# Kernel tuning notes

Hardware: AMD Instinct MI355X
Metric: run time of the kernel (lower is better)

The kernel has to match this reference:

```python
import jax, jax.numpy as jnp
import numpy as np

H = 16
D_MODEL = 1024
D_K = D_MODEL // H
NWORDS = 16384


def setup_inputs() -> dict:
    key0 = jax.random.key(0)
    ks = jax.random.split(key0, 11)
    s = 0.02
    return {
        "query": jax.random.normal(ks[0], (1, D_MODEL), dtype=jnp.float32),
        "key": jax.random.normal(ks[1], (NWORDS, D_MODEL), dtype=jnp.float32),
        "value": jax.random.normal(ks[2], (NWORDS, D_MODEL), dtype=jnp.float32),
        "Wq": jax.random.normal(ks[3], (D_MODEL, D_MODEL), dtype=jnp.float32) * s,
        "bq": jax.random.normal(ks[4], (D_MODEL,), dtype=jnp.float32) * s,
        "Wk": jax.random.normal(ks[5], (D_MODEL, D_MODEL), dtype=jnp.float32) * s,
        "bk": jax.random.normal(ks[6], (D_MODEL,), dtype=jnp.float32) * s,
        "Wv": jax.random.normal(ks[7], (D_MODEL, D_MODEL), dtype=jnp.float32) * s,
        "bv": jax.random.normal(ks[8], (D_MODEL,), dtype=jnp.float32) * s,
        "Wo": jax.random.normal(ks[9], (D_MODEL, D_MODEL), dtype=jnp.float32) * s,
        "bo": jax.random.normal(ks[10], (D_MODEL,), dtype=jnp.float32) * s,
    }


def reference(query, key, value, Wq, bq, Wk, bk, Wv, bv, Wo, bo):
    # torch Linear: y = x @ W.T + b
    q = (query @ Wq.T + bq).reshape(H, D_K)          # [h, d_k]  (single query token)
    k = (key @ Wk.T + bk).reshape(-1, H, D_K)        # [n, h, d_k]
    v = (value @ Wv.T + bv).reshape(-1, H, D_K)      # [n, h, d_k]
    # NOTE: original module applies NO 1/sqrt(d_k) scaling.
    scores = jnp.einsum("hd,nhd->hn", q, k)          # [h, n]
    p_attn = jax.nn.softmax(scores, axis=-1)          # dropout p=0 -> no-op
    x = jnp.einsum("hn,nhd->hd", p_attn, v).reshape(1, H * D_K)  # [1, d_model]
    return x @ Wo.T + bo                              # [1, d_model]
```

## Files before the change

kernel.cpp:

```cpp
#include <hip/hip_runtime.h>

#define DM 1024
#define NW 16384

typedef __attribute__((ext_vector_type(8))) short short8;
typedef __attribute__((ext_vector_type(4))) float f32x4;

#define OFF_AH   1024
#define OFF_AL   9216
#define OFF_D0   17408
#define OFF_S    17424
#define OFF_X    17696
#define OFF_W    18720
#define OFF_E    36864
#define OFF_PART 299008

__device__ __forceinline__ unsigned short f2bf(float f) {
  unsigned int u = __float_as_uint(f);
  return (unsigned short)((u + 0x7fffu + ((u >> 16) & 1u)) >> 16);
}

__global__ __launch_bounds__(256) void k_rowdot(const float* __restrict__ W,
                                                const float* __restrict__ v,
                                                const float* __restrict__ b,
                                                float* __restrict__ out) {
  const int wave = (blockIdx.x * 256 + threadIdx.x) >> 6;
  const int lane = threadIdx.x & 63;
  const float* row = W + (size_t)wave * DM + 4 * lane;
  float s = 0.f;
#pragma unroll
  for (int j = 0; j < 4; ++j) {
    float4 a = *(const float4*)(row + j * 256);
    float4 x = *(const float4*)(v + j * 256 + 4 * lane);
    s += a.x * x.x + a.y * x.y + a.z * x.z + a.w * x.w;
  }
#pragma unroll
  for (int off = 32; off; off >>= 1) s += __shfl_xor(s, off, 64);
  if (lane == 0) out[wave] = s + b[wave];
}

__global__ __launch_bounds__(256) void k_qck(const float* __restrict__ Wq,
                                             const float* __restrict__ bq,
                                             const float* __restrict__ query,
                                             const float* __restrict__ Wk,
                                             const float* __restrict__ bk,
                                             short* __restrict__ Ah,
                                             short* __restrict__ Al,
                                             float* __restrict__ d0,
                                             float* __restrict__ S) {
  const int h = blockIdx.x >> 2;
  const int mc = blockIdx.x & 3;
  const int t = threadIdx.x;
  const int lane = t & 63;
  const int wv = t >> 6;
  __shared__ float qh[64];
  if (blockIdx.x == 0 && t < 16) S[t * 16] = 0.f;
  float4 qv[4];
#pragma unroll
  for (int j = 0; j < 4; ++j) qv[j] = *(const float4*)(query + j * 256 + 4 * lane);
#pragma unroll 1
  for (int i = 0; i < 16; i += 2) {
    const int d0i = 4 * i + wv;
    const int d1i = 4 * (i + 1) + wv;
    const float* r0 = Wq + (size_t)(h * 64 + d0i) * DM + 4 * lane;
    const float* r1 = Wq + (size_t)(h * 64 + d1i) * DM + 4 * lane;
    float4 a0[4], a1[4];
#pragma unroll
    for (int j = 0; j < 4; ++j) { a0[j] = *(const float4*)(r0 + j * 256);
                                  a1[j] = *(const float4*)(r1 + j * 256); }
    float s0 = 0.f, s1 = 0.f;
#pragma unroll
    for (int j = 0; j < 4; ++j) {
      s0 += a0[j].x * qv[j].x + a0[j].y * qv[j].y + a0[j].z * qv[j].z + a0[j].w * qv[j].w;
      s1 += a1[j].x * qv[j].x + a1[j].y * qv[j].y + a1[j].z * qv[j].z + a1[j].w * qv[j].w;
    }
#pragma unroll
    for (int off = 32; off; off >>= 1) { s0 += __shfl_xor(s0, off, 64);
                                         s1 += __shfl_xor(s1, off, 64); }
    if (lane == 0) { qh[d0i] = s0 + bq[h * 64 + d0i];
                     qh[d1i] = s1 + bq[h * 64 + d1i]; }
  }
  __syncthreads();
  const int m = mc * 256 + t;
  const float* Wp = Wk + (size_t)(h * 64) * DM + m;
  float s = 0.f;
#pragma unroll 1
  for (int db = 0; db < 8; ++db) {
    float wv8[8];
#pragma unroll
    for (int j = 0; j < 8; ++j) wv8[j] = Wp[(size_t)(db * 8 + j) * DM];
#pragma unroll
    for (int j = 0; j < 8; ++j) s = fmaf(qh[db * 8 + j], wv8[j], s);
  }
  unsigned short hu = f2bf(s);
  float hf = __uint_as_float(((unsigned int)hu) << 16);
  unsigned short lu = f2bf(s - hf);
  const int kb = m >> 5, q = (m >> 3) & 3, j = m & 7;
  const int idx = (kb * 64 + q * 16 + h) * 8 + j;
  Ah[idx] = (short)hu;
  Al[idx] = (short)lu;
  if (mc == 0 && t == 0) {
    float tt = 0.f;
    for (int d = 0; d < 64; ++d) tt += qh[d] * bk[h * 64 + d];
    d0[h] = tt;
  }
}

__global__ __launch_bounds__(512) void k_scores(const float* __restrict__ key,
                                                const short* __restrict__ AhG,
                                                const short* __restrict__ AlG,
                                                const float* __restrict__ d0,
                                                float* __restrict__ e,
                                                float* __restrict__ S) {
  const int t = threadIdx.x;
  const int lane = t & 63;
  const int wv = t >> 6;
  const int tile = blockIdx.x;
  const int n = tile * 16 + (lane & 15);
  const int quad = lane >> 4;
  const int kb0 = wv * 4;
  const float* base = key + (size_t)n * DM + quad * 8;
  const short8* A8h = (const short8*)AhG;
  const short8* A8l = (const short8*)AlG;

  short8 ah[4], al[4];
  float4 f0[4], f1[4];
#pragma unroll
  for (int i = 0; i < 4; ++i) {
    ah[i] = A8h[(kb0 + i) * 64 + lane];
    al[i] = A8l[(kb0 + i) * 64 + lane];
    f0[i] = *(const float4*)(base + (kb0 + i) * 32);
    f1[i] = *(const float4*)(base + (kb0 + i) * 32 + 4);
  }
  f32x4 acc = {0.f, 0.f, 0.f, 0.f};
#pragma unroll
  for (int i = 0; i < 4; ++i) {
    float ff[8] = {f0[i].x, f0[i].y, f0[i].z, f0[i].w,
                   f1[i].x, f1[i].y, f1[i].z, f1[i].w};
    short8 bh, bl;
#pragma unroll
    for (int j = 0; j < 8; ++j) {
      unsigned short hu = f2bf(ff[j]);
      bh[j] = (short)hu;
      float hf = __uint_as_float(((unsigned int)hu) << 16);
      bl[j] = (short)f2bf(ff[j] - hf);
    }
    acc = __builtin_amdgcn_mfma_f32_16x16x32_bf16(ah[i], bh, acc, 0, 0, 0);
    acc = __builtin_amdgcn_mfma_f32_16x16x32_bf16(ah[i], bl, acc, 0, 0, 0);
    acc = __builtin_amdgcn_mfma_f32_16x16x32_bf16(al[i], bh, acc, 0, 0, 0);
  }
  __shared__ float4 red[8][64];
  red[wv][lane] = make_float4(acc[0], acc[1], acc[2], acc[3]);
  __syncthreads();
  if (wv == 0) {
    float4 a = red[0][lane];
#pragma unroll
    for (int w = 1; w < 8; ++w) {
      float4 o = red[w][lane];
      a.x += o.x; a.y += o.y; a.z += o.z; a.w += o.w;
    }
    const float4 dv = *(const float4*)(d0 + quad * 4);
    float ex0 = __expf(a.x + dv.x);
    float ex1 = __expf(a.y + dv.y);
    float ex2 = __expf(a.z + dv.z);
    float ex3 = __expf(a.w + dv.w);
    *(float4*)(e + (size_t)n * 16 + quad * 4) = make_float4(ex0, ex1, ex2, ex3);
    float sr[4] = {ex0, ex1, ex2, ex3};
#pragma unroll
    for (int r = 0; r < 4; ++r) {
      float v = sr[r];
      v += __shfl_xor(v, 1, 64);
      v += __shfl_xor(v, 2, 64);
      v += __shfl_xor(v, 4, 64);
      v += __shfl_xor(v, 8, 64);
      if ((lane & 15) == 0) atomicAdd(S + (size_t)(quad * 4 + r) * 16, v);
    }
  }
}

__global__ __launch_bounds__(256, 2) void k_pv(const float* __restrict__ value,
                                               const float* __restrict__ e,
                                               float* __restrict__ part) {
  const int nb = blockIdx.x >> 2;
  const int mc = blockIdx.x & 3;
  const int t = threadIdx.x;
  const int lane = t & 63;
  const int wy = t >> 6;
  const int col = mc * 256 + lane * 4;
  const int n0 = nb * 256;
  __shared__ float el[256 * 16];
  __shared__ float4 red[2][16][64];
  {
    const float4* eg = (const float4*)(e + (size_t)n0 * 16);
    float4* es = (float4*)el;
#pragma unroll
    for (int k = 0; k < 4; ++k) es[t + k * 256] = eg[t + k * 256];
  }
  __syncthreads();
  float4 acc[16];
#pragma unroll
  for (int h = 0; h < 16; ++h) acc[h] = make_float4(0.f, 0.f, 0.f, 0.f);
  const float* vp = value + (size_t)(n0 + wy * 64) * DM + col;
  const float* ep = &el[wy * 64 * 16];
#pragma unroll 1
  for (int rb = 0; rb < 8; ++rb) {
    float4 v[8];
#pragma unroll
    for (int i = 0; i < 8; ++i) v[i] = *(const float4*)(vp + (size_t)(rb * 8 + i) * DM);
#pragma unroll
    for (int i = 0; i < 8; ++i) {
      const float4* er4 = (const float4*)(ep + (rb * 8 + i) * 16);
      float4 e0 = er4[0], e1 = er4[1], e2 = er4[2], e3 = er4[3];
      float4 vv = v[i];
#define FMA4H(H, P) { acc[H].x = fmaf(P, vv.x, acc[H].x); acc[H].y = fmaf(P, vv.y, acc[H].y); \
                      acc[H].z = fmaf(P, vv.z, acc[H].z); acc[H].w = fmaf(P, vv.w, acc[H].w); }
      FMA4H(0,  e0.x) FMA4H(1,  e0.y) FMA4H(2,  e0.z) FMA4H(3,  e0.w)
      FMA4H(4,  e1.x) FMA4H(5,  e1.y) FMA4H(6,  e1.z) FMA4H(7,  e1.w)
      FMA4H(8,  e2.x) FMA4H(9,  e2.y) FMA4H(10, e2.z) FMA4H(11, e2.w)
      FMA4H(12, e3.x) FMA4H(13, e3.y) FMA4H(14, e3.z) FMA4H(15, e3.w)
#undef FMA4H
    }
  }
  if (wy >= 2) {
#pragma unroll
    for (int h = 0; h < 16; ++h) red[wy - 2][h][lane] = acc[h];
  }
  __syncthreads();
  if (wy < 2) {
#pragma unroll
    for (int h = 0; h < 16; ++h) {
      float4 o = red[wy][h][lane];
      acc[h].x += o.x; acc[h].y += o.y; acc[h].z += o.z; acc[h].w += o.w;
    }
  }
  __syncthreads();
  if (wy == 1) {
#pragma unroll
    for (int h = 0; h < 16; ++h) red[0][h][lane] = acc[h];
  }
  __syncthreads();
  if (wy == 0) {
    float* pp = part + (size_t)nb * (16 * DM) + col;
#pragma unroll
    for (int h = 0; h < 16; ++h) {
      float4 o = red[0][h][lane];
      acc[h].x += o.x; acc[h].y += o.y; acc[h].z += o.z; acc[h].w += o.w;
      *(float4*)(pp + (size_t)h * DM) = acc[h];
    }
  }
}

__global__ __launch_bounds__(256) void k_wred(const float* __restrict__ part,
                                              float* __restrict__ w) {
  const int gid = blockIdx.x * 256 + threadIdx.x;
  const int o = gid >> 2;
  const int q = gid & 3;
  float s = 0.f;
#pragma unroll 1
  for (int ib = 0; ib < 2; ++ib) {
    float x[8];
#pragma unroll
    for (int j = 0; j < 8; ++j) x[j] = part[(size_t)(q * 16 + ib * 8 + j) * 16384 + o];
#pragma unroll
    for (int j = 0; j < 8; ++j) s += x[j];
  }
  s += __shfl_xor(s, 1, 64);
  s += __shfl_xor(s, 2, 64);
  if (q == 0) w[o] = s;
}

__global__ __launch_bounds__(256) void k_xproj(const float* __restrict__ Wv,
                                               const float* __restrict__ w,
                                               const float* __restrict__ bv,
                                               const float* __restrict__ S,
                                               float* __restrict__ x) {
  const int wave = (blockIdx.x * 256 + threadIdx.x) >> 6;
  const int lane = threadIdx.x & 63;
  const int h = wave >> 6;
  const float* vec = w + (size_t)h * DM;
  const float* row = Wv + (size_t)wave * DM + 4 * lane;
  float s = 0.f;
#pragma unroll
  for (int j = 0; j < 4; ++j) {
    float4 a = *(const float4*)(row + j * 256);
    float4 x4 = *(const float4*)(vec + j * 256 + 4 * lane);
    s += a.x * x4.x + a.y * x4.y + a.z * x4.z + a.w * x4.w;
  }
#pragma unroll
  for (int off = 32; off; off >>= 1) s += __shfl_xor(s, off, 64);
  if (lane == 0) x[wave] = s / S[(size_t)h * 16] + bv[wave];
}

extern "C" void kernel_launch(void* const* d_in, const int* in_sizes, int n_in,
                              void* d_out, int out_size, void* d_ws, size_t ws_size,
                              hipStream_t stream) {
  const float* query = (const float*)d_in[0];
  const float* key   = (const float*)d_in[1];
  const float* value = (const float*)d_in[2];
  const float* Wq    = (const float*)d_in[3];
  const float* bq    = (const float*)d_in[4];
  const float* Wk    = (const float*)d_in[5];
  const float* bk    = (const float*)d_in[6];
  const float* Wv    = (const float*)d_in[7];
  const float* bv    = (const float*)d_in[8];
  const float* Wo    = (const float*)d_in[9];
  const float* bo    = (const float*)d_in[10];
  float* out = (float*)d_out;
  float* ws  = (float*)d_ws;
  short* Ah  = (short*)(ws + OFF_AH);
  short* Al  = (short*)(ws + OFF_AL);

  k_qck    <<<64,  256, 0, stream>>>(Wq, bq, query, Wk, bk, Ah, Al, ws + OFF_D0, ws + OFF_S);
  k_scores <<<1024,512, 0, stream>>>(key, Ah, Al, ws + OFF_D0, ws + OFF_E, ws + OFF_S);
  k_pv     <<<256, 256, 0, stream>>>(value, ws + OFF_E, ws + OFF_PART);
  k_wred   <<<256, 256, 0, stream>>>(ws + OFF_PART, ws + OFF_W);
  k_xproj  <<<256, 256, 0, stream>>>(Wv, ws + OFF_W, bv, ws + OFF_S, ws + OFF_X);
  k_rowdot <<<256, 256, 0, stream>>>(Wo, ws + OFF_X, bo, out);
}
```

Measured before the change: 237.4 us.

## Restructure score kernel to one wave per tile and move softmax sum into PV

k_scores now runs one wave per 16-row tile. Each wave walks all 32 k-blocks with double-buffered register loads and two independent MFMA accumulators, which removes the LDS cross-wave reduction and the per-tile atomics. The softmax denominator is now summed in k_pv from the exp values already staged in shared memory, and S becomes a contiguous array. k_pv uses 128-row chunks across 512 blocks, and k_wred now reduces 128 partials. The trade-off is far fewer waves in flight for the bandwidth-bound key read, plus double the partial-sum buffer size.

Measured after the change: 216.2 us. -8.9%, faster.

```diff
diff --git a/kernel.cpp b/kernel.cpp
--- a/kernel.cpp
+++ b/kernel.cpp
@@ -54,7 +54,7 @@
   const int lane = t & 63;
   const int wv = t >> 6;
   __shared__ float qh[64];
-  if (blockIdx.x == 0 && t < 16) S[t * 16] = 0.f;
+  if (blockIdx.x == 0 && t < 16) S[t] = 0.f;
   float4 qv[4];
 #pragma unroll
   for (int j = 0; j < 4; ++j) qv[j] = *(const float4*)(query + j * 256 + 4 * lane);
@@ -106,104 +106,116 @@
   }
 }
 
-__global__ __launch_bounds__(512) void k_scores(const float* __restrict__ key,
-                                                const short* __restrict__ AhG,
-                                                const short* __restrict__ AlG,
-                                                const float* __restrict__ d0,
-                                                float* __restrict__ e,
-                                                float* __restrict__ S) {
-  const int t = threadIdx.x;
-  const int lane = t & 63;
-  const int wv = t >> 6;
+__global__ __launch_bounds__(64, 1) void k_scores(const float* __restrict__ key,
+                                                  const short* __restrict__ AhG,
+                                                  const short* __restrict__ AlG,
+                                                  const float* __restrict__ d0,
+                                                  float* __restrict__ e) {
   const int tile = blockIdx.x;
+  const int lane = threadIdx.x;
   const int n = tile * 16 + (lane & 15);
   const int quad = lane >> 4;
-  const int kb0 = wv * 4;
   const float* base = key + (size_t)n * DM + quad * 8;
   const short8* A8h = (const short8*)AhG;
   const short8* A8l = (const short8*)AlG;
 
-  short8 ah[4], al[4];
-  float4 f0[4], f1[4];
-#pragma unroll
-  for (int i = 0; i < 4; ++i) {
-    ah[i] = A8h[(kb0 + i) * 64 + lane];
-    al[i] = A8l[(kb0 + i) * 64 + lane];
-    f0[i] = *(const float4*)(base + (kb0 + i) * 32);
-    f1[i] = *(const float4*)(base + (kb0 + i) * 32 + 4);
-  }
-  f32x4 acc = {0.f, 0.f, 0.f, 0.f};
-#pragma unroll
-  for (int i = 0; i < 4; ++i) {
-    float ff[8] = {f0[i].x, f0[i].y, f0[i].z, f0[i].w,
-                   f1[i].x, f1[i].y, f1[i].z, f1[i].w};
-    short8 bh, bl;
-#pragma unroll
-    for (int j = 0; j < 8; ++j) {
-      unsigned short hu = f2bf(ff[j]);
-      bh[j] = (short)hu;
-      float hf = __uint_as_float(((unsigned int)hu) << 16);
-      bl[j] = (short)f2bf(ff[j] - hf);
-    }
-    acc = __builtin_amdgcn_mfma_f32_16x16x32_bf16(ah[i], bh, acc, 0, 0, 0);
-    acc = __builtin_amdgcn_mfma_f32_16x16x32_bf16(ah[i], bl, acc, 0, 0, 0);
-    acc = __builtin_amdgcn_mfma_f32_16x16x32_bf16(al[i], bh, acc, 0, 0, 0);
-  }
-  __shared__ float4 red[8][64];
-  red[wv][lane] = make_float4(acc[0], acc[1], acc[2], acc[3]);
-  __syncthreads();
-  if (wv == 0) {
-    float4 a = red[0][lane];
-#pragma unroll
-    for (int w = 1; w < 8; ++w) {
-      float4 o = red[w][lane];
-      a.x += o.x; a.y += o.y; a.z += o.z; a.w += o.w;
-    }
-    const float4 dv = *(const float4*)(d0 + quad * 4);
-    float ex0 = __expf(a.x + dv.x);
-    float ex1 = __expf(a.y + dv.y);
-    float ex2 = __expf(a.z + dv.z);
-    float ex3 = __expf(a.w + dv.w);
-    *(float4*)(e + (size_t)n * 16 + quad * 4) = make_float4(ex0, ex1, ex2, ex3);
-    float sr[4] = {ex0, ex1, ex2, ex3};
-#pragma unroll
-    for (int r = 0; r < 4; ++r) {
-      float v = sr[r];
-      v += __shfl_xor(v, 1, 64);
-      v += __shfl_xor(v, 2, 64);
-      v += __shfl_xor(v, 4, 64);
-      v += __shfl_xor(v, 8, 64);
-      if ((lane & 15) == 0) atomicAdd(S + (size_t)(quad * 4 + r) * 16, v);
-    }
-  }
+  short8 ah[2][4], al[2][4];
+  float4 f0[2][4], f1[2][4];
+  f32x4 acc0 = {0.f, 0.f, 0.f, 0.f};
+  f32x4 acc1 = {0.f, 0.f, 0.f, 0.f};
+
+#define LOADG(buf, g) { \
+  _Pragma("unroll") for (int i = 0; i < 4; ++i) { \
+    const int kb = (g) * 4 + i; \
+    ah[buf][i] = A8h[kb * 64 + lane]; \
+    al[buf][i] = A8l[kb * 64 + lane]; \
+    f0[buf][i] = *(const float4*)(base + kb * 32); \
+    f1[buf][i] = *(const float4*)(base + kb * 32 + 4); \
+  } }
+
+#define PROC(buf) { \
+  _Pragma("unroll") for (int i = 0; i < 4; ++i) { \
+    float ff[8] = {f0[buf][i].x, f0[buf][i].y, f0[buf][i].z, f0[buf][i].w, \
+                   f1[buf][i].x, f1[buf][i].y, f1[buf][i].z, f1[buf][i].w}; \
+    short8 bh, bl; \
+    _Pragma("unroll") for (int j = 0; j < 8; ++j) { \
+      unsigned short hu = f2bf(ff[j]); \
+      bh[j] = (short)hu; \
+      float hf = __uint_as_float(((unsigned int)hu) << 16); \
+      bl[j] = (short)f2bf(ff[j] - hf); \
+    } \
+    if ((i & 1) == 0) { \
+      acc0 = __builtin_amdgcn_mfma_f32_16x16x32_bf16(ah[buf][i], bh, acc0, 0, 0, 0); \
+      acc0 = __builtin_amdgcn_mfma_f32_16x16x32_bf16(ah[buf][i], bl, acc0, 0, 0, 0); \
+      acc0 = __builtin_amdgcn_mfma_f32_16x16x32_bf16(al[buf][i], bh, acc0, 0, 0, 0); \
+    } else { \
+      acc1 = __builtin_amdgcn_mfma_f32_16x16x32_bf16(ah[buf][i], bh, acc1, 0, 0, 0); \
+      acc1 = __builtin_amdgcn_mfma_f32_16x16x32_bf16(ah[buf][i], bl, acc1, 0, 0, 0); \
+      acc1 = __builtin_amdgcn_mfma_f32_16x16x32_bf16(al[buf][i], bh, acc1, 0, 0, 0); \
+    } \
+  } }
+
+  LOADG(0, 0)
+  LOADG(1, 1)
+  PROC(0) LOADG(0, 2)
+  PROC(1) LOADG(1, 3)
+  PROC(0) LOADG(0, 4)
+  PROC(1) LOADG(1, 5)
+  PROC(0) LOADG(0, 6)
+  PROC(1) LOADG(1, 7)
+  PROC(0)
+  PROC(1)
+#undef LOADG
+#undef PROC
+
+  const float4 dv = *(const float4*)(d0 + quad * 4);
+  float ex0 = __expf(acc0[0] + acc1[0] + dv.x);
+  float ex1 = __expf(acc0[1] + acc1[1] + dv.y);
+  float ex2 = __expf(acc0[2] + acc1[2] + dv.z);
+  float ex3 = __expf(acc0[3] + acc1[3] + dv.w);
+  *(float4*)(e + (size_t)n * 16 + quad * 4) = make_float4(ex0, ex1, ex2, ex3);
 }
 
 __global__ __launch_bounds__(256, 2) void k_pv(const float* __restrict__ value,
                                                const float* __restrict__ e,
-                                               float* __restrict__ part) {
+                                               float* __restrict__ part,
+                                               float* __restrict__ S) {
   const int nb = blockIdx.x >> 2;
   const int mc = blockIdx.x & 3;
   const int t = threadIdx.x;
   const int lane = t & 63;
   const int wy = t >> 6;
   const int col = mc * 256 + lane * 4;
-  const int n0 = nb * 256;
-  __shared__ float el[256 * 16];
+  const int n0 = nb * 128;
+  __shared__ float el[128 * 16];
   __shared__ float4 red[2][16][64];
+  __shared__ float sp[4][16];
   {
     const float4* eg = (const float4*)(e + (size_t)n0 * 16);
     float4* es = (float4*)el;
 #pragma unroll
-    for (int k = 0; k < 4; ++k) es[t + k * 256] = eg[t + k * 256];
-  }
-  __syncthreads();
+    for (int k = 0; k < 2; ++k) es[t + k * 256] = eg[t + k * 256];
+  }
+  __syncthreads();
+  if (mc == 0) {
+    const int h = t & 15;
+    const int rg = t >> 4;
+    float p = 0.f;
+#pragma unroll
+    for (int j = 0; j < 8; ++j) p += el[(rg * 8 + j) * 16 + h];
+    p += __shfl_xor(p, 16, 64);
+    p += __shfl_xor(p, 32, 64);
+    if (lane < 16) sp[wy][lane] = p;
+    __syncthreads();
+    if (t < 16) atomicAdd(S + t, sp[0][t] + sp[1][t] + sp[2][t] + sp[3][t]);
+  }
   float4 acc[16];
 #pragma unroll
   for (int h = 0; h < 16; ++h) acc[h] = make_float4(0.f, 0.f, 0.f, 0.f);
-  const float* vp = value + (size_t)(n0 + wy * 64) * DM + col;
-  const float* ep = &el[wy * 64 * 16];
+  const float* vp = value + (size_t)(n0 + wy * 32) * DM + col;
+  const float* ep = &el[wy * 32 * 16];
 #pragma unroll 1
-  for (int rb = 0; rb < 8; ++rb) {
+  for (int rb = 0; rb < 4; ++rb) {
     float4 v[8];
 #pragma unroll
     for (int i = 0; i < 8; ++i) v[i] = *(const float4*)(vp + (size_t)(rb * 8 + i) * DM);
@@ -256,11 +268,11 @@
   const int o = gid >> 2;
   const int q = gid & 3;
   float s = 0.f;
-#pragma unroll 1
-  for (int ib = 0; ib < 2; ++ib) {
+#pragma unroll
+  for (int ib = 0; ib < 4; ++ib) {
     float x[8];
 #pragma unroll
-    for (int j = 0; j < 8; ++j) x[j] = part[(size_t)(q * 16 + ib * 8 + j) * 16384 + o];
+    for (int j = 0; j < 8; ++j) x[j] = part[(size_t)(q * 32 + ib * 8 + j) * 16384 + o];
 #pragma unroll
     for (int j = 0; j < 8; ++j) s += x[j];
   }
@@ -288,7 +300,7 @@
   }
 #pragma unroll
   for (int off = 32; off; off >>= 1) s += __shfl_xor(s, off, 64);
-  if (lane == 0) x[wave] = s / S[(size_t)h * 16] + bv[wave];
+  if (lane == 0) x[wave] = s / S[h] + bv[wave];
 }
 
 extern "C" void kernel_launch(void* const* d_in, const int* in_sizes, int n_in,
@@ -311,8 +323,8 @@
   short* Al  = (short*)(ws + OFF_AL);
 
   k_qck    <<<64,  256, 0, stream>>>(Wq, bq, query, Wk, bk, Ah, Al, ws + OFF_D0, ws + OFF_S);
-  k_scores <<<1024,512, 0, stream>>>(key, Ah, Al, ws + OFF_D0, ws + OFF_E, ws + OFF_S);
-  k_pv     <<<256, 256, 0, stream>>>(value, ws + OFF_E, ws + OFF_PART);
+  k_scores <<<1024, 64, 0, stream>>>(key, Ah, Al, ws + OFF_D0, ws + OFF_E);
+  k_pv     <<<512, 256, 0, stream>>>(value, ws + OFF_E, ws + OFF_PART, ws + OFF_S);
   k_wred   <<<256, 256, 0, stream>>>(ws + OFF_PART, ws + OFF_W);
   k_xproj  <<<256, 256, 0, stream>>>(Wv, ws + OFF_W, bv, ws + OFF_S, ws + OFF_X);
   k_rowdot <<<256, 256, 0, stream>>>(Wo, ws + OFF_X, bo, out);
```
